# Optimization experiments

Measured on AMD Instinct MI355X. Metric: run time of the kernel, lower is better.

## Reference

```python
import jax, jax.numpy as jnp
import numpy as np
from jax import lax

D = 1024
DI = 2 * D          # mamba inner dim
NS = 16             # ssm state size
DTR = D // 16       # dt rank = 64
KC = 4              # conv kernel
E = 8               # experts
DFF = 2 * D         # expert hidden
TOPK = 2


def _ln(x, g, b):
    mu = x.mean(-1, keepdims=True)
    var = ((x - mu) ** 2).mean(-1, keepdims=True)
    return (x - mu) * lax.rsqrt(var + 1e-5) * g + b


def _silu(x):
    return x * jax.nn.sigmoid(x)


def setup_inputs() -> dict:
    key = jax.random.key(0)
    ks = jax.random.split(key, 20)
    s = 0.02
    inp = {
        "x": jax.random.normal(ks[0], (2, 2048, D), jnp.float32),
        # layernorms
        "ln_mamba_g": jnp.ones((D,), jnp.float32),
        "ln_mamba_b": jnp.zeros((D,), jnp.float32),
        "ln_moe_g": jnp.ones((D,), jnp.float32),
        "ln_moe_b": jnp.zeros((D,), jnp.float32),
        # mamba params
        "in_proj_w": jax.random.normal(ks[1], (2 * DI, D), jnp.float32) * s,
        "in_proj_b": jnp.zeros((2 * DI,), jnp.float32),
        "conv_w": jax.random.normal(ks[2], (DI, KC), jnp.float32) * s,
        "conv_b": jnp.zeros((DI,), jnp.float32),
        "x_proj_w": jax.random.normal(ks[3], (DTR + 2 * NS, DI), jnp.float32) * s,
        "dt_proj_w": jax.random.normal(ks[4], (DI, DTR), jnp.float32) * s,
        "dt_proj_b": jnp.full((DI,), -4.6, jnp.float32),  # softplus -> small dt
        "A_log": jnp.log(jnp.broadcast_to(jnp.arange(1, NS + 1, dtype=jnp.float32), (DI, NS))),
        "D_skip": jnp.ones((DI,), jnp.float32),
        "out_proj_w": jax.random.normal(ks[5], (D, DI), jnp.float32) * s,
        # moe params
        "router_w": jax.random.normal(ks[6], (E, D), jnp.float32) * s,
        "w1": jax.random.normal(ks[7], (E, DFF, D), jnp.float32) * s,
        "b1": jnp.zeros((E, DFF), jnp.float32),
        "w2": jax.random.normal(ks[8], (E, D, DFF), jnp.float32) * s,
        "b2": jnp.zeros((E, D), jnp.float32),
    }
    return inp


def _mamba(x, in_proj_w, in_proj_b, conv_w, conv_b, x_proj_w,
           dt_proj_w, dt_proj_b, A_log, D_skip, out_proj_w):
    Bz, T, _ = x.shape
    xz = x @ in_proj_w.T + in_proj_b            # [B,T,2*DI]
    xi, z = xz[..., :DI], xz[..., DI:]
    # causal depthwise conv, kernel 4
    xp = jnp.pad(xi, ((0, 0), (KC - 1, 0), (0, 0)))
    xc = conv_b + sum(conv_w[:, k] * xp[:, k:k + T, :] for k in range(KC))
    xc = _silu(xc)                              # [B,T,DI]
    proj = xc @ x_proj_w.T                      # [B,T,DTR+2*NS]
    dt_r = proj[..., :DTR]
    Bm = proj[..., DTR:DTR + NS]                # [B,T,NS]
    Cm = proj[..., DTR + NS:]                   # [B,T,NS]
    dt = jax.nn.softplus(dt_r @ dt_proj_w.T + dt_proj_b)  # [B,T,DI]
    A = -jnp.exp(A_log)                         # [DI,NS]

    def step(h, inp):
        xt, dtt, Bt, Ct = inp                   # [B,DI],[B,DI],[B,NS],[B,NS]
        dA = jnp.exp(dtt[:, :, None] * A)       # [B,DI,NS]
        h = dA * h + (dtt * xt)[:, :, None] * Bt[:, None, :]
        y = jnp.einsum('bdn,bn->bd', h, Ct)
        return h, y

    h0 = jnp.zeros((Bz, DI, NS), x.dtype)
    xs = (xc.transpose(1, 0, 2), dt.transpose(1, 0, 2),
          Bm.transpose(1, 0, 2), Cm.transpose(1, 0, 2))
    _, ys = lax.scan(step, h0, xs)              # [T,B,DI]
    y = ys.transpose(1, 0, 2) + xc * D_skip
    y = y * _silu(z)
    return y @ out_proj_w.T                     # [B,T,D]


def _moe(x, router_w, w1, b1, w2, b2):
    logits = x @ router_w.T                     # [B,T,E]
    probs = jax.nn.softmax(logits, axis=-1)
    topv, topi = lax.top_k(probs, TOPK)
    topv = topv / topv.sum(-1, keepdims=True)
    w = (jax.nn.one_hot(topi, E, dtype=x.dtype) * topv[..., None]).sum(-2)  # [B,T,E]
    out = jnp.zeros_like(x)
    for e in range(E):                          # fixed small expert loop
        h1 = _silu(x @ w1[e].T + b1[e])
        ye = h1 @ w2[e].T + b2[e]
        out = out + w[..., e:e + 1] * ye
    return out, {"router_probs": probs}


def reference(x, ln_mamba_g, ln_mamba_b, ln_moe_g, ln_moe_b,
              in_proj_w, in_proj_b, conv_w, conv_b, x_proj_w,
              dt_proj_w, dt_proj_b, A_log, D_skip, out_proj_w,
              router_w, w1, b1, w2, b2):
    h_norm = _ln(x, ln_mamba_g, ln_mamba_b)
    mamba_out = _mamba(h_norm, in_proj_w, in_proj_b, conv_w, conv_b, x_proj_w,
                       dt_proj_w, dt_proj_b, A_log, D_skip, out_proj_w)
    h = x + mamba_out
    h_moe_in = _ln(h, ln_moe_g, ln_moe_b)
    moe_delta, aux = _moe(h_moe_in, router_w, w1, b1, w2, b2)
    h = h + moe_delta
    return (h, aux["router_probs"])
```

## Files before the change

kernel.cpp:

```cpp
#include <hip/hip_runtime.h>
#include <hip/hip_bf16.h>
#include <math.h>

#define NTOK   4096
#define TSEQ   2048
#define DMODEL 1024
#define DINNER 2048
#define NSTATE 16
#define DTRANK 64
#define NEXP   8
#define DFF    2048
#define NCHUNK 32
#define CLEN   64

typedef __attribute__((ext_vector_type(8))) short short8;
typedef __attribute__((ext_vector_type(4))) float f32x4;

__device__ __forceinline__ float fast_rcp(float x){ return __builtin_amdgcn_rcpf(x); }
__device__ __forceinline__ float siluf(float x){ return x * fast_rcp(1.f + __expf(-x)); }

__device__ __forceinline__ unsigned short f2bf(float x){
  unsigned int u = __float_as_uint(x);
  unsigned int r = (u + 0x7FFFu + ((u >> 16) & 1u)) >> 16;
  return (unsigned short)r;
}

__device__ __forceinline__ void split4(float4 a, unsigned short* hi, unsigned short* lo){
  float av[4] = {a.x, a.y, a.z, a.w};
  #pragma unroll
  for (int j=0;j<4;j++){
    unsigned short hu = f2bf(av[j]);
    float hf = __uint_as_float((unsigned int)hu << 16);
    hi[j] = hu;
    lo[j] = f2bf(av[j] - hf);
  }
}

__global__ void zero_kernel(int* __restrict__ p){ p[threadIdx.x] = 0; }

__global__ __launch_bounds__(256) void split_kernel(
    const float* __restrict__ in, unsigned short* __restrict__ hi,
    unsigned short* __restrict__ lo, int n)
{
  int i = (blockIdx.x*256 + threadIdx.x)*4;
  if (i >= n) return;
  float4 v = *(const float4*)(in + i);
  unsigned short ht[4], lt[4];
  split4(v, ht, lt);
  uint2 hw, lw;
  hw.x = (unsigned)ht[0] | ((unsigned)ht[1]<<16);
  hw.y = (unsigned)ht[2] | ((unsigned)ht[3]<<16);
  lw.x = (unsigned)lt[0] | ((unsigned)lt[1]<<16);
  lw.y = (unsigned)lt[2] | ((unsigned)lt[3]<<16);
  *(uint2*)(hi+i) = hw;
  *(uint2*)(lo+i) = lw;
}

__global__ __launch_bounds__(256) void cvt_bf_kernel(
    const float* __restrict__ in, unsigned short* __restrict__ out, int n)
{
  int i = (blockIdx.x*256 + threadIdx.x)*8;
  if (i >= n) return;
  float4 a = *(const float4*)(in+i);
  float4 b = *(const float4*)(in+i+4);
  short8 v;
  v[0]=(short)f2bf(a.x); v[1]=(short)f2bf(a.y); v[2]=(short)f2bf(a.z); v[3]=(short)f2bf(a.w);
  v[4]=(short)f2bf(b.x); v[5]=(short)f2bf(b.y); v[6]=(short)f2bf(b.z); v[7]=(short)f2bf(b.w);
  *(short8*)(out+i) = v;
}

template<int EPI, int BM, bool PS, int CT, bool SK>
__global__ __launch_bounds__(256) void gemm_big(
    const float* __restrict__ A,
    const unsigned short* __restrict__ Ahi, const unsigned short* __restrict__ Alo, int lda,
    const unsigned short* __restrict__ Whi, const unsigned short* __restrict__ Wlo, int ldw,
    int M, int N, int K,
    const float* __restrict__ bias,
    float* __restrict__ out, int ldo)
{
  constexpr int BN  = CT*16;
  constexpr int RG  = BM/64;
  constexpr int TPR = 256/BM;
  constexpr int EA  = 32/TPR;
  constexpr int TPW = 256/BN;
  constexpr int EW  = 32/TPW;
  const int tid = threadIdx.x;
  const int m0 = blockIdx.y * BM;
  const int n0 = blockIdx.x * BN;
  const int koff = SK ? blockIdx.z * K : 0;
  float* outp = out + (SK ? (size_t)blockIdx.z * M * ldo : 0);

  __shared__ __align__(16) unsigned short Ahs[BM*40];
  __shared__ __align__(16) unsigned short Als[BM*40];
  __shared__ __align__(16) unsigned short Whs[BN*40];
  __shared__ __align__(16) unsigned short Wls[BN*40];

  const int arow = tid / TPR;
  const int aseg = (tid % TPR) * EA;
  const int wrow = tid / TPW;
  const int wseg = (tid % TPW) * EW;

  const float* Ap = PS ? nullptr : (A + (size_t)(m0 + arow)*lda + aseg + koff);
  const unsigned short* Aph = PS ? (Ahi + (size_t)(m0 + arow)*lda + aseg + koff) : nullptr;
  const unsigned short* Apl = PS ? (Alo + (size_t)(m0 + arow)*lda + aseg + koff) : nullptr;
  const bool wok = (n0 + wrow) < N;
  const unsigned short* Whp = Whi + (size_t)(n0 + wrow)*ldw + wseg + koff;
  const unsigned short* Wlp = Wlo + (size_t)(n0 + wrow)*ldw + wseg + koff;

  const int lane = tid & 63;
  const int wv   = tid >> 6;
  const int qd   = lane >> 4;
  const int mr   = lane & 15;

  f32x4 acc[RG][CT];
  #pragma unroll
  for (int rg=0; rg<RG; rg++)
    #pragma unroll
    for (int ct=0; ct<CT; ct++) acc[rg][ct] = (f32x4){0.f,0.f,0.f,0.f};

  const unsigned short* ardh = &Ahs[(wv*(16*RG) + mr)*40 + qd*8];
  const unsigned short* ardl = &Als[(wv*(16*RG) + mr)*40 + qd*8];
  const unsigned short* brdh = &Whs[mr*40 + qd*8];
  const unsigned short* brdl = &Wls[mr*40 + qd*8];

  const short8 z8 = {0,0,0,0,0,0,0,0};

  for (int kt = 0; kt < K; kt += 32){
    short8 ah[EA/8], al[EA/8];
    if (PS){
      #pragma unroll
      for (int h=0; h<EA/8; h++){
        ah[h] = *(const short8*)(Aph + kt + h*8);
        al[h] = *(const short8*)(Apl + kt + h*8);
      }
    } else {
      #pragma unroll
      for (int q=0; q<EA/4; q++){
        float4 f = *(const float4*)(Ap + kt + q*4);
        unsigned short ht[4], lt[4];
        split4(f, ht, lt);
        #pragma unroll
        for (int j=0;j<4;j++){
          ah[(q*4+j)/8][(q*4+j)&7] = (short)ht[j];
          al[(q*4+j)/8][(q*4+j)&7] = (short)lt[j];
        }
      }
    }
    short8 wh[EW/8], wl[EW/8];
    #pragma unroll
    for (int h=0; h<EW/8; h++){
      wh[h] = wok ? *(const short8*)(Whp + kt + h*8) : z8;
      wl[h] = wok ? *(const short8*)(Wlp + kt + h*8) : z8;
    }
    __syncthreads();
    #pragma unroll
    for (int h=0; h<EA/8; h++){
      *(short8*)&Ahs[arow*40 + aseg + h*8] = ah[h];
      *(short8*)&Als[arow*40 + aseg + h*8] = al[h];
    }
    #pragma unroll
    for (int h=0; h<EW/8; h++){
      *(short8*)&Whs[wrow*40 + wseg + h*8] = wh[h];
      *(short8*)&Wls[wrow*40 + wseg + h*8] = wl[h];
    }
    __syncthreads();
    #pragma unroll
    for (int rg=0; rg<RG; rg++){
      short8 af = *(const short8*)(ardh + rg*16*40);
      short8 alf= *(const short8*)(ardl + rg*16*40);
      #pragma unroll
      for (int ct=0; ct<CT; ct++){
        short8 bh = *(const short8*)(brdh + ct*16*40);
        short8 bl = *(const short8*)(brdl + ct*16*40);
        f32x4 t = acc[rg][ct];
        t = __builtin_amdgcn_mfma_f32_16x16x32_bf16(af, bh, t, 0,0,0);
        t = __builtin_amdgcn_mfma_f32_16x16x32_bf16(alf, bh, t, 0,0,0);
        t = __builtin_amdgcn_mfma_f32_16x16x32_bf16(af, bl, t, 0,0,0);
        acc[rg][ct] = t;
      }
    }
  }

  #pragma unroll
  for (int rg=0; rg<RG; rg++){
    #pragma unroll
    for (int ct=0; ct<CT; ct++){
      int colg = n0 + ct*16 + mr;
      if (colg >= N) continue;
      float bias_v = (EPI==0 || EPI==2) ? bias[colg] : 0.f;
      #pragma unroll
      for (int r=0;r<4;r++){
        int rowg = m0 + wv*(16*RG) + rg*16 + qd*4 + r;
        float v = acc[rg][ct][r];
        if (EPI == 0){ v += bias_v; }
        else if (EPI == 2){ v += bias_v; v = (v > 20.f) ? v : log1pf(expf(v)); }
        outp[(size_t)rowg*ldo + colg] = v;
      }
    }
  }
}

__global__ __launch_bounds__(256) void reduce4_kernel(
    const float* __restrict__ pp, float* __restrict__ out, int n)
{
  int i = (blockIdx.x*256 + threadIdx.x)*4;
  if (i >= n) return;
  float4 a = *(const float4*)(pp + i);
  float4 b = *(const float4*)(pp + n + i);
  float4 c = *(const float4*)(pp + 2*(size_t)n + i);
  float4 d = *(const float4*)(pp + 3*(size_t)n + i);
  float4 o;
  o.x = (a.x+b.x)+(c.x+d.x);
  o.y = (a.y+b.y)+(c.y+d.y);
  o.z = (a.z+b.z)+(c.z+d.z);
  o.w = (a.w+b.w)+(c.w+d.w);
  *(float4*)(out + i) = o;
}

__global__ __launch_bounds__(256) void reduce2r_kernel(
    const float* __restrict__ p0, const float* __restrict__ p1,
    const float* __restrict__ r, float* __restrict__ out, int n)
{
  int i = (blockIdx.x*256 + threadIdx.x)*4;
  if (i >= n) return;
  float4 a = *(const float4*)(p0 + i);
  float4 b = *(const float4*)(p1 + i);
  float4 c = *(const float4*)(r + i);
  float4 o;
  o.x = a.x+b.x+c.x; o.y = a.y+b.y+c.y; o.z = a.z+b.z+c.z; o.w = a.w+b.w+c.w;
  *(float4*)(out + i) = o;
}

__global__ __launch_bounds__(256) void ln_split_kernel(
    const float* __restrict__ x, const float* __restrict__ g, const float* __restrict__ b,
    unsigned short* __restrict__ hi, unsigned short* __restrict__ lo)
{
  int tok = blockIdx.x;
  int tid = threadIdx.x;
  const float* row = x + (size_t)tok * DMODEL;
  float v[4];
  float s = 0.f, sq = 0.f;
  #pragma unroll
  for (int j=0;j<4;j++){
    v[j] = row[j*256 + tid];
    s += v[j]; sq += v[j]*v[j];
  }
  #pragma unroll
  for (int o=1;o<64;o<<=1){ s += __shfl_xor(s,o,64); sq += __shfl_xor(sq,o,64); }
  __shared__ float ss[4], ssq[4];
  int wid = tid >> 6, lane = tid & 63;
  if (lane == 0){ ss[wid]=s; ssq[wid]=sq; }
  __syncthreads();
  s  = ss[0]+ss[1]+ss[2]+ss[3];
  sq = ssq[0]+ssq[1]+ssq[2]+ssq[3];
  float mu = s * (1.f/DMODEL);
  float var = sq * (1.f/DMODEL) - mu*mu;
  float rs = rsqrtf(var + 1e-5f);
  #pragma unroll
  for (int j=0;j<4;j++){
    int d = j*256 + tid;
    float o = (v[j]-mu)*rs*g[d] + b[d];
    unsigned short hu = f2bf(o);
    float hf = __uint_as_float((unsigned int)hu << 16);
    hi[(size_t)tok*DMODEL + d] = hu;
    lo[(size_t)tok*DMODEL + d] = f2bf(o - hf);
  }
}

__global__ __launch_bounds__(256) void ln2_kernel(
    const float* __restrict__ x, const float* __restrict__ g, const float* __restrict__ b,
    float* __restrict__ out, unsigned short* __restrict__ outb)
{
  int tok = blockIdx.x;
  int tid = threadIdx.x;
  const float* row = x + (size_t)tok * DMODEL;
  float v[4];
  float s = 0.f, sq = 0.f;
  #pragma unroll
  for (int j=0;j<4;j++){
    v[j] = row[j*256 + tid];
    s += v[j]; sq += v[j]*v[j];
  }
  #pragma unroll
  for (int o=1;o<64;o<<=1){ s += __shfl_xor(s,o,64); sq += __shfl_xor(sq,o,64); }
  __shared__ float ss[4], ssq[4];
  int wid = tid >> 6, lane = tid & 63;
  if (lane == 0){ ss[wid]=s; ssq[wid]=sq; }
  __syncthreads();
  s  = ss[0]+ss[1]+ss[2]+ss[3];
  sq = ssq[0]+ssq[1]+ssq[2]+ssq[3];
  float mu = s * (1.f/DMODEL);
  float var = sq * (1.f/DMODEL) - mu*mu;
  float rs = rsqrtf(var + 1e-5f);
  #pragma unroll
  for (int j=0;j<4;j++){
    int d = j*256 + tid;
    float o = (v[j]-mu)*rs*g[d] + b[d];
    out[(size_t)tok*DMODEL + d] = o;
    outb[(size_t)tok*DMODEL + d] = f2bf(o);
  }
}

__global__ __launch_bounds__(256) void conv_kernel(
    const float* __restrict__ xz, const float* __restrict__ cw,
    const float* __restrict__ cb, float* __restrict__ xc)
{
  int i = blockIdx.x*256 + threadIdx.x;
  int tok = i >> 11;
  int ch  = i & 2047;
  int t   = tok & (TSEQ-1);
  int b   = tok >> 11;
  float acc = cb[ch];
  #pragma unroll
  for (int k=0;k<4;k++){
    int tt = t + k - 3;
    if (tt >= 0)
      acc = fmaf(cw[ch*4 + k], xz[(size_t)((b<<11)+tt)*4096 + ch], acc);
  }
  xc[i] = siluf(acc);
}

__global__ __launch_bounds__(256) void scan_partial(
    const float* __restrict__ xz, const float* __restrict__ xc,
    const float* __restrict__ proj, const float* __restrict__ A_log,
    float* __restrict__ P, float* __restrict__ Q)
{
  int tid = threadIdx.x;
  int ch  = blockIdx.x*256 + tid;
  int c   = blockIdx.y;
  int b   = blockIdx.z;
  float A[16];
  #pragma unroll
  for (int n=0;n<16;n++) A[n] = -expf(A_log[ch*NSTATE + n]);
  float h[16];
  #pragma unroll
  for (int n=0;n<16;n++) h[n] = 0.f;
  float sdt = 0.f;
  int tok0 = (b<<11) + c*CLEN;
  float dtv = xz[(size_t)tok0*4096 + ch];
  float xt  = xc[(size_t)tok0*2048 + ch];
  for (int i=0;i<CLEN;i++){
    int tn = tok0 + ((i+1 < CLEN) ? i+1 : i);
    float dtv_n = xz[(size_t)tn*4096 + ch];
    float xt_n  = xc[(size_t)tn*2048 + ch];
    const float4* pB = (const float4*)(proj + (size_t)(tok0+i)*96 + 64);
    float Bv[16];
    *(float4*)&Bv[0]  = pB[0];
    *(float4*)&Bv[4]  = pB[1];
    *(float4*)&Bv[8]  = pB[2];
    *(float4*)&Bv[12] = pB[3];
    float dxt = dtv*xt;
    sdt += dtv;
    #pragma unroll
    for (int n=0;n<16;n++){
      float dA = __expf(dtv*A[n]);
      h[n] = fmaf(dA, h[n], dxt*Bv[n]);
    }
    dtv = dtv_n; xt = xt_n;
  }
  size_t base = ((((size_t)(b*NCHUNK + c))<<11 | ch)<<4);
  #pragma unroll
  for (int n=0;n<16;n++){
    P[base+n] = __expf(A[n]*sdt);
    Q[base+n] = h[n];
  }
}

__global__ __launch_bounds__(256) void scan_combine(
    const float* __restrict__ Q, float* PH)
{
  int g = blockIdx.x*256 + threadIdx.x;
  int n = g & 15, ch = (g>>4) & 2047, b = g>>15;
  float hs = 0.f;
  for (int c=0;c<NCHUNK;c++){
    size_t idx = ((((size_t)(b*NCHUNK + c))<<11 | ch)<<4) | n;
    float pv = PH[idx];
    float qv = Q[idx];
    PH[idx] = hs;
    hs = fmaf(pv, hs, qv);
  }
}

__global__ __launch_bounds__(256) void scan_final(
    const float* __restrict__ xz, float* __restrict__ xc,
    const float* __restrict__ proj, const float* __restrict__ A_log,
    const float* __restrict__ Dskip, const float* __restrict__ Hs)
{
  int tid = threadIdx.x;
  int ch  = blockIdx.x*256 + tid;
  int c   = blockIdx.y;
  int b   = blockIdx.z;
  float A[16];
  #pragma unroll
  for (int n=0;n<16;n++) A[n] = -expf(A_log[ch*NSTATE + n]);
  float Dv = Dskip[ch];
  size_t base = ((((size_t)(b*NCHUNK + c))<<11 | ch)<<4);
  float h[16];
  #pragma unroll
  for (int n=0;n<16;n++) h[n] = Hs[base+n];
  int tok0 = (b<<11) + c*CLEN;
  float dtv = xz[(size_t)tok0*4096 + ch];
  float xt  = xc[(size_t)tok0*2048 + ch];
  float zv  = xz[(size_t)tok0*4096 + 2048 + ch];
  for (int i=0;i<CLEN;i++){
    int tn = tok0 + ((i+1 < CLEN) ? i+1 : i);
    float dtv_n = xz[(size_t)tn*4096 + ch];
    float xt_n  = xc[(size_t)tn*2048 + ch];
    float zv_n  = xz[(size_t)tn*4096 + 2048 + ch];
    const float4* pB = (const float4*)(proj + (size_t)(tok0+i)*96 + 64);
    float Bv[16], Cv[16];
    *(float4*)&Bv[0]  = pB[0];
    *(float4*)&Bv[4]  = pB[1];
    *(float4*)&Bv[8]  = pB[2];
    *(float4*)&Bv[12] = pB[3];
    *(float4*)&Cv[0]  = pB[4];
    *(float4*)&Cv[4]  = pB[5];
    *(float4*)&Cv[8]  = pB[6];
    *(float4*)&Cv[12] = pB[7];
    float dxt = dtv*xt;
    float y = xt*Dv;
    #pragma unroll
    for (int n=0;n<16;n++){
      float dA = __expf(dtv*A[n]);
      h[n] = fmaf(dA, h[n], dxt*Bv[n]);
      y = fmaf(h[n], Cv[n], y);
    }
    xc[(size_t)(tok0+i)*2048 + ch] = y * siluf(zv);
    dtv = dtv_n; xt = xt_n; zv = zv_n;
  }
}

__global__ __launch_bounds__(256) void router_kernel(
    const float* __restrict__ hmoe, const float* __restrict__ rw,
    float* __restrict__ probs_out, int* __restrict__ cnt,
    int* __restrict__ tok_e0, int* __restrict__ tok_e1,
    float* __restrict__ tok_w0, float* __restrict__ tok_w1)
{
  int tok = blockIdx.x;
  int tid = threadIdx.x;
  int e = tid >> 5, l = tid & 31;
  float s = 0.f;
  const float* row = hmoe + (size_t)tok*DMODEL;
  const float* wr  = rw + (size_t)e*DMODEL;
  for (int d=l; d<DMODEL; d+=32) s = fmaf(row[d], wr[d], s);
  #pragma unroll
  for (int o=1;o<32;o<<=1) s += __shfl_xor(s,o,64);
  __shared__ float lg[8];
  if (l==0) lg[e]=s;
  __syncthreads();
  if (tid==0){
    float mx = lg[0];
    for (int k=1;k<8;k++) mx = fmaxf(mx, lg[k]);
    float pe[8]; float den=0.f;
    for (int k=0;k<8;k++){ pe[k]=expf(lg[k]-mx); den+=pe[k]; }
    float inv = 1.f/den;
    for (int k=0;k<8;k++) probs_out[tok*8+k] = pe[k]*inv;
    int i0=0;
    for (int k=1;k<8;k++) if (pe[k] > pe[i0]) i0=k;
    int i1 = (i0==0)?1:0;
    for (int k=0;k<8;k++) if (k!=i0 && pe[k] > pe[i1]) i1=k;
    float v0=pe[i0], v1=pe[i1], sw=v0+v1;
    tok_e0[tok]=i0; tok_e1[tok]=i1;
    tok_w0[tok]=v0/sw; tok_w1[tok]=v1/sw;
    atomicAdd(&cnt[i0],1); atomicAdd(&cnt[i1],1);
  }
}

__global__ void prefix_kernel(const int* cnt, int* off, int* fill){
  if (threadIdx.x==0){
    int s=0;
    for (int e=0;e<NEXP;e++){ off[e]=s; s+=cnt[e]; fill[e]=0; }
  }
}

__global__ __launch_bounds__(256) void fill_kernel(
    const int* tok_e0, const int* tok_e1, const float* tok_w0, const float* tok_w1,
    const int* off, int* fill, int* slot_tok, float* slot_w)
{
  int tok = blockIdx.x*256 + threadIdx.x;
  int e0=tok_e0[tok], e1=tok_e1[tok];
  int p0 = atomicAdd(&fill[e0],1); int s0 = off[e0]+p0;
  slot_tok[s0]=tok; slot_w[s0]=tok_w0[tok];
  int p1 = atomicAdd(&fill[e1],1); int s1 = off[e1]+p1;
  slot_tok[s1]=tok; slot_w[s1]=tok_w1[tok];
}

__global__ __launch_bounds__(256) void moe_gemm1(
    const unsigned short* __restrict__ hnb, const unsigned short* __restrict__ w1b,
    const float* __restrict__ b1,
    const int* __restrict__ cnt, const int* __restrict__ off,
    const int* __restrict__ slot_tok, unsigned short* __restrict__ H1)
{
  int e = blockIdx.z;
  int c = cnt[e];
  int r0 = blockIdx.y*128;
  if (r0 >= c) return;
  int base = off[e];
  int tid = threadIdx.x;
  __shared__ int toks[128];
  if (tid < 128) toks[tid] = (r0 + tid < c) ? slot_tok[base + r0 + tid] : -1;
  __shared__ __align__(16) unsigned short As[128*40];
  __shared__ __align__(16) unsigned short Ws[128*40];
  __syncthreads();

  const int n0   = blockIdx.x*128;
  const int srow = tid >> 1;
  const int sseg = (tid & 1) * 16;
  const int tok  = toks[srow];
  const bool aok = (tok >= 0);
  const unsigned short* Ap = hnb + (size_t)(aok ? tok : 0)*DMODEL + sseg;
  const unsigned short* Wp = w1b + (size_t)e*DFF*DMODEL + (size_t)(n0+srow)*DMODEL + sseg;

  const int lane = tid & 63;
  const int wv   = tid >> 6;
  const int qd   = lane >> 4;
  const int mr   = lane & 15;

  f32x4 acc[2][8];
  #pragma unroll
  for (int rg=0; rg<2; rg++)
    #pragma unroll
    for (int ct=0; ct<8; ct++) acc[rg][ct] = (f32x4){0.f,0.f,0.f,0.f};

  const unsigned short* ard = &As[(wv*32 + mr)*40 + qd*8];
  const unsigned short* brd = &Ws[mr*40 + qd*8];
  const short8 z8 = {0,0,0,0,0,0,0,0};

  for (int kt = 0; kt < DMODEL; kt += 32){
    short8 a0 = aok ? *(const short8*)(Ap + kt)     : z8;
    short8 a1 = aok ? *(const short8*)(Ap + kt + 8) : z8;
    short8 w0 = *(const short8*)(Wp + kt);
    short8 w1v= *(const short8*)(Wp + kt + 8);
    __syncthreads();
    *(short8*)&As[srow*40 + sseg]     = a0;
    *(short8*)&As[srow*40 + sseg + 8] = a1;
    *(short8*)&Ws[srow*40 + sseg]     = w0;
    *(short8*)&Ws[srow*40 + sseg + 8] = w1v;
    __syncthreads();
    #pragma unroll
    for (int rg=0; rg<2; rg++){
      short8 af = *(const short8*)(ard + rg*16*40);
      #pragma unroll
      for (int ct=0; ct<8; ct++){
        short8 bf = *(const short8*)(brd + ct*16*40);
        acc[rg][ct] = __builtin_amdgcn_mfma_f32_16x16x32_bf16(af, bf, acc[rg][ct], 0,0,0);
      }
    }
  }

  #pragma unroll
  for (int rg=0; rg<2; rg++){
    #pragma unroll
    for (int ct=0; ct<8; ct++){
      int colg = n0 + ct*16 + mr;
      float bias = b1[(size_t)e*DFF + colg];
      #pragma unroll
      for (int r=0;r<4;r++){
        int sl = wv*32 + rg*16 + qd*4 + r;
        if (toks[sl] < 0) continue;
        float v = acc[rg][ct][r] + bias;
        H1[(size_t)(base + r0 + sl)*DFF + colg] = f2bf(siluf(v));
      }
    }
  }
}

__global__ __launch_bounds__(256) void moe_gemm2(
    const unsigned short* __restrict__ H1, const unsigned short* __restrict__ w2b,
    const float* __restrict__ b2,
    const int* __restrict__ cnt, const int* __restrict__ off,
    const int* __restrict__ slot_tok, const float* __restrict__ slot_w,
    float* __restrict__ hres)
{
  int e = blockIdx.z;
  int c = cnt[e];
  int r0 = blockIdx.y*128;
  if (r0 >= c) return;
  int base = off[e];
  int tid = threadIdx.x;
  __shared__ int toks[128];
  __shared__ float wts[128];
  if (tid < 128){
    int r = r0 + tid;
    toks[tid] = (r<c) ? slot_tok[base+r] : -1;
    wts[tid]  = (r<c) ? slot_w[base+r] : 0.f;
  }
  __shared__ __align__(16) unsigned short As[128*40];
  __shared__ __align__(16) unsigned short Ws[128*40];
  __syncthreads();

  const int n0   = blockIdx.x*128;
  const int srow = tid >> 1;
  const int sseg = (tid & 1) * 16;
  const bool aok = (toks[srow] >= 0);
  const unsigned short* Ap = H1 + (size_t)(base + r0 + (aok ? srow : 0))*DFF + sseg;
  const unsigned short* Wp = w2b + (size_t)e*DMODEL*DFF + (size_t)(n0+srow)*DFF + sseg;

  const int lane = tid & 63;
  const int wv   = tid >> 6;
  const int qd   = lane >> 4;
  const int mr   = lane & 15;

  f32x4 acc[2][8];
  #pragma unroll
  for (int rg=0; rg<2; rg++)
    #pragma unroll
    for (int ct=0; ct<8; ct++) acc[rg][ct] = (f32x4){0.f,0.f,0.f,0.f};

  const unsigned short* ard = &As[(wv*32 + mr)*40 + qd*8];
  const unsigned short* brd = &Ws[mr*40 + qd*8];
  const short8 z8 = {0,0,0,0,0,0,0,0};

  for (int kt = 0; kt < DFF; kt += 32){
    short8 a0 = aok ? *(const short8*)(Ap + kt)     : z8;
    short8 a1 = aok ? *(const short8*)(Ap + kt + 8) : z8;
    short8 w0 = *(const short8*)(Wp + kt);
    short8 w1v= *(const short8*)(Wp + kt + 8);
    __syncthreads();
    *(short8*)&As[srow*40 + sseg]     = a0;
    *(short8*)&As[srow*40 + sseg + 8] = a1;
    *(short8*)&Ws[srow*40 + sseg]     = w0;
    *(short8*)&Ws[srow*40 + sseg + 8] = w1v;
    __syncthreads();
    #pragma unroll
    for (int rg=0; rg<2; rg++){
      short8 af = *(const short8*)(ard + rg*16*40);
      #pragma unroll
      for (int ct=0; ct<8; ct++){
        short8 bf = *(const short8*)(brd + ct*16*40);
        acc[rg][ct] = __builtin_amdgcn_mfma_f32_16x16x32_bf16(af, bf, acc[rg][ct], 0,0,0);
      }
    }
  }

  #pragma unroll
  for (int rg=0; rg<2; rg++){
    #pragma unroll
    for (int ct=0; ct<8; ct++){
      int colg = n0 + ct*16 + mr;
      float bias = b2[(size_t)e*DMODEL + colg];
      #pragma unroll
      for (int r=0;r<4;r++){
        int sl = wv*32 + rg*16 + qd*4 + r;
        int t = toks[sl];
        if (t < 0) continue;
        float v = acc[rg][ct][r] + bias;
        atomicAdd(&hres[(size_t)t*DMODEL + colg], wts[sl]*v);
      }
    }
  }
}

extern "C" void kernel_launch(void* const* d_in, const int* in_sizes, int n_in,
                              void* d_out, int out_size, void* d_ws, size_t ws_size,
                              hipStream_t stream)
{
  const float* x         = (const float*)d_in[0];
  const float* ln_m_g    = (const float*)d_in[1];
  const float* ln_m_b    = (const float*)d_in[2];
  const float* ln_e_g    = (const float*)d_in[3];
  const float* ln_e_b    = (const float*)d_in[4];
  const float* in_proj_w = (const float*)d_in[5];
  const float* in_proj_b = (const float*)d_in[6];
  const float* conv_w    = (const float*)d_in[7];
  const float* conv_b    = (const float*)d_in[8];
  const float* x_proj_w  = (const float*)d_in[9];
  const float* dt_proj_w = (const float*)d_in[10];
  const float* dt_proj_b = (const float*)d_in[11];
  const float* A_log     = (const float*)d_in[12];
  const float* D_skip    = (const float*)d_in[13];
  const float* out_proj_w= (const float*)d_in[14];
  const float* router_w  = (const float*)d_in[15];
  const float* w1        = (const float*)d_in[16];
  const float* b1        = (const float*)d_in[17];
  const float* w2        = (const float*)d_in[18];
  const float* b2        = (const float*)d_in[19];

  char* ws = (char*)d_ws;
  float* xz   = (float*)(ws + 0);
  float* xc   = (float*)(ws + 67108864ull);
  float* proj = (float*)(ws + 100663296ull);
  char*  misc = ws + 102236160ull;
  float* hn   = (float*)(ws + 0);
  float* pout = (float*)(ws + 16777216ull);
  unsigned short* H1    = (unsigned short*)(ws + 16777216ull);
  unsigned short* hn_bf = (unsigned short*)(ws + 50331648ull);
  unsigned short* wmoe  = (unsigned short*)(ws + 67108864ull);

  unsigned short* hn_hi = (unsigned short*)d_out;
  unsigned short* hn_lo = hn_hi + 4194304;
  float* Pbuf = (float*)d_out;
  float* Qbuf = (float*)d_out + (2u<<20);
  float* ppx  = (float*)((char*)d_out + 2097152ull);

  unsigned short* Wi_hi = (unsigned short*)(ws + 67108864ull);
  unsigned short* Wi_lo = Wi_hi + 4194304;
  unsigned short* Wo_hi = (unsigned short*)Qbuf;
  unsigned short* Wo_lo = Wo_hi + 2097152;
  unsigned short* Wx_hi = (unsigned short*)d_out;
  unsigned short* Wx_lo = Wx_hi + 196608;
  unsigned short* Wd_hi = Wx_lo + 196608;
  unsigned short* Wd_lo = Wd_hi + 131072;

  int*   cnt      = (int*)(misc);
  int*   fill     = (int*)(misc + 64);
  int*   offp     = (int*)(misc + 128);
  int*   tok_e0   = (int*)(misc + 1024);
  int*   tok_e1   = (int*)(misc + 1024 + 16384);
  float* tok_w0   = (float*)(misc + 1024 + 32768);
  float* tok_w1   = (float*)(misc + 1024 + 49152);
  int*   slot_tok = (int*)(misc + 1024 + 65536);
  float* slot_w   = (float*)(misc + 1024 + 98304);
  float* out_h    = (float*)d_out;
  float* probs_out= (float*)d_out + 4194304;

  zero_kernel<<<1, 64, 0, stream>>>(cnt);

  split_kernel<<<4096, 256, 0, stream>>>(in_proj_w, Wi_hi, Wi_lo, 4194304);
  ln_split_kernel<<<NTOK, 256, 0, stream>>>(x, ln_m_g, ln_m_b, hn_hi, hn_lo);
  gemm_big<0,128,true,8,false><<<dim3(32, 32), 256, 0, stream>>>(
      nullptr, hn_hi, hn_lo, DMODEL, Wi_hi, Wi_lo, DMODEL, NTOK, 4096, DMODEL,
      in_proj_b, xz, 4096);
  split_kernel<<<192, 256, 0, stream>>>(x_proj_w, Wx_hi, Wx_lo, 196608);
  split_kernel<<<128, 256, 0, stream>>>(dt_proj_w, Wd_hi, Wd_lo, 131072);
  conv_kernel<<<NTOK*DINNER/256, 256, 0, stream>>>(xz, conv_w, conv_b, xc);
  gemm_big<1,64,false,8,true><<<dim3(1, 64, 4), 256, 0, stream>>>(
      xc, nullptr, nullptr, DINNER, Wx_hi, Wx_lo, DINNER, NTOK, 96, 512,
      nullptr, ppx, 96);
  reduce4_kernel<<<384, 256, 0, stream>>>(ppx, proj, NTOK*96);
  gemm_big<2,128,false,8,false><<<dim3(16, 32), 256, 0, stream>>>(
      proj, nullptr, nullptr, 96, Wd_hi, Wd_lo, DTRANK, NTOK, DINNER, DTRANK,
      dt_proj_b, xz, 4096);
  scan_partial<<<dim3(DINNER/256, NCHUNK, 2), 256, 0, stream>>>(
      xz, xc, proj, A_log, Pbuf, Qbuf);
  scan_combine<<<256, 256, 0, stream>>>(Qbuf, Pbuf);
  scan_final<<<dim3(DINNER/256, NCHUNK, 2), 256, 0, stream>>>(
      xz, xc, proj, A_log, D_skip, Pbuf);
  split_kernel<<<2048, 256, 0, stream>>>(out_proj_w, Wo_hi, Wo_lo, 2097152);
  gemm_big<1,128,false,8,true><<<dim3(8, 32, 2), 256, 0, stream>>>(
      xc, nullptr, nullptr, DINNER, Wo_hi, Wo_lo, DINNER, NTOK, DMODEL, 1024,
      nullptr, pout, DMODEL);
  reduce2r_kernel<<<4096, 256, 0, stream>>>(pout, pout + 4194304, x, out_h,
                                            NTOK*DMODEL);

  ln2_kernel<<<NTOK, 256, 0, stream>>>(out_h, ln_e_g, ln_e_b, hn, hn_bf);
  router_kernel<<<NTOK, 256, 0, stream>>>(hn, router_w, probs_out, cnt,
                                          tok_e0, tok_e1, tok_w0, tok_w1);
  prefix_kernel<<<1, 64, 0, stream>>>(cnt, offp, fill);
  fill_kernel<<<NTOK/256, 256, 0, stream>>>(tok_e0, tok_e1, tok_w0, tok_w1,
                                            offp, fill, slot_tok, slot_w);
  cvt_bf_kernel<<<8192, 256, 0, stream>>>(w1, wmoe, NEXP*DFF*DMODEL);
  moe_gemm1<<<dim3(DFF/128, 32, NEXP), 256, 0, stream>>>(
      hn_bf, wmoe, b1, cnt, offp, slot_tok, H1);
  cvt_bf_kernel<<<8192, 256, 0, stream>>>(w2, wmoe, NEXP*DMODEL*DFF);
  moe_gemm2<<<dim3(DMODEL/128, 32, NEXP), 256, 0, stream>>>(
      H1, wmoe, b2, cnt, offp, slot_tok, slot_w, out_h);
}
```

Baseline: 968.0 us.

## Double-buffer shared-memory tiles in dense and MoE GEMM kernels

Converts the main GEMM and both MoE expert GEMM kernels from single-buffered LDS tiles to double buffering. The next K-tile's global loads are issued before the MFMA loop on the current tile and stored into the alternate buffer afterwards, which cuts one barrier per iteration. This is meant to hide global-load latency behind matrix math. In exchange it doubles LDS per block and keeps the prefetched registers live across the MFMA loop, which can lower occupancy.

```diff
diff --git a/kernel.cpp b/kernel.cpp
--- a/kernel.cpp
+++ b/kernel.cpp
@@ -84,16 +84,18 @@
   constexpr int EA  = 32/TPR;
   constexpr int TPW = 256/BN;
   constexpr int EW  = 32/TPW;
+  constexpr int AH  = BM*40;
+  constexpr int WH  = BN*40;
   const int tid = threadIdx.x;
   const int m0 = blockIdx.y * BM;
   const int n0 = blockIdx.x * BN;
   const int koff = SK ? blockIdx.z * K : 0;
   float* outp = out + (SK ? (size_t)blockIdx.z * M * ldo : 0);
 
-  __shared__ __align__(16) unsigned short Ahs[BM*40];
-  __shared__ __align__(16) unsigned short Als[BM*40];
-  __shared__ __align__(16) unsigned short Whs[BN*40];
-  __shared__ __align__(16) unsigned short Wls[BN*40];
+  __shared__ __align__(16) unsigned short Ahs[2*AH];
+  __shared__ __align__(16) unsigned short Als[2*AH];
+  __shared__ __align__(16) unsigned short Whs[2*WH];
+  __shared__ __align__(16) unsigned short Wls[2*WH];
 
   const int arow = tid / TPR;
   const int aseg = (tid % TPR) * EA;
@@ -118,15 +120,13 @@
     #pragma unroll
     for (int ct=0; ct<CT; ct++) acc[rg][ct] = (f32x4){0.f,0.f,0.f,0.f};
 
-  const unsigned short* ardh = &Ahs[(wv*(16*RG) + mr)*40 + qd*8];
-  const unsigned short* ardl = &Als[(wv*(16*RG) + mr)*40 + qd*8];
-  const unsigned short* brdh = &Whs[mr*40 + qd*8];
-  const unsigned short* brdl = &Wls[mr*40 + qd*8];
-
+  const int ard_o = (wv*(16*RG) + mr)*40 + qd*8;
+  const int brd_o = mr*40 + qd*8;
   const short8 z8 = {0,0,0,0,0,0,0,0};
 
-  for (int kt = 0; kt < K; kt += 32){
-    short8 ah[EA/8], al[EA/8];
+  short8 ah[EA/8], al[EA/8], wh[EW/8], wl[EW/8];
+
+  auto load_tile = [&](int kt){
     if (PS){
       #pragma unroll
       for (int h=0; h<EA/8; h++){
@@ -146,32 +146,41 @@
         }
       }
     }
-    short8 wh[EW/8], wl[EW/8];
     #pragma unroll
     for (int h=0; h<EW/8; h++){
       wh[h] = wok ? *(const short8*)(Whp + kt + h*8) : z8;
       wl[h] = wok ? *(const short8*)(Wlp + kt + h*8) : z8;
     }
-    __syncthreads();
+  };
+  auto store_tile = [&](int b){
     #pragma unroll
     for (int h=0; h<EA/8; h++){
-      *(short8*)&Ahs[arow*40 + aseg + h*8] = ah[h];
-      *(short8*)&Als[arow*40 + aseg + h*8] = al[h];
+      *(short8*)&Ahs[b*AH + arow*40 + aseg + h*8] = ah[h];
+      *(short8*)&Als[b*AH + arow*40 + aseg + h*8] = al[h];
     }
     #pragma unroll
     for (int h=0; h<EW/8; h++){
-      *(short8*)&Whs[wrow*40 + wseg + h*8] = wh[h];
-      *(short8*)&Wls[wrow*40 + wseg + h*8] = wl[h];
-    }
-    __syncthreads();
+      *(short8*)&Whs[b*WH + wrow*40 + wseg + h*8] = wh[h];
+      *(short8*)&Wls[b*WH + wrow*40 + wseg + h*8] = wl[h];
+    }
+  };
+
+  load_tile(0);
+  store_tile(0);
+  __syncthreads();
+
+  int cur = 0;
+  for (int kt = 0; kt < K; kt += 32){
+    const bool hn = (kt + 32 < K);
+    if (hn) load_tile(kt + 32);
     #pragma unroll
     for (int rg=0; rg<RG; rg++){
-      short8 af = *(const short8*)(ardh + rg*16*40);
-      short8 alf= *(const short8*)(ardl + rg*16*40);
+      short8 af = *(const short8*)&Ahs[cur*AH + ard_o + rg*16*40];
+      short8 alf= *(const short8*)&Als[cur*AH + ard_o + rg*16*40];
       #pragma unroll
       for (int ct=0; ct<CT; ct++){
-        short8 bh = *(const short8*)(brdh + ct*16*40);
-        short8 bl = *(const short8*)(brdl + ct*16*40);
+        short8 bh = *(const short8*)&Whs[cur*WH + brd_o + ct*16*40];
+        short8 bl = *(const short8*)&Wls[cur*WH + brd_o + ct*16*40];
         f32x4 t = acc[rg][ct];
         t = __builtin_amdgcn_mfma_f32_16x16x32_bf16(af, bh, t, 0,0,0);
         t = __builtin_amdgcn_mfma_f32_16x16x32_bf16(alf, bh, t, 0,0,0);
@@ -179,6 +188,9 @@
         acc[rg][ct] = t;
       }
     }
+    if (hn) store_tile(cur ^ 1);
+    __syncthreads();
+    cur ^= 1;
   }
 
   #pragma unroll
@@ -499,8 +511,8 @@
   int tid = threadIdx.x;
   __shared__ int toks[128];
   if (tid < 128) toks[tid] = (r0 + tid < c) ? slot_tok[base + r0 + tid] : -1;
-  __shared__ __align__(16) unsigned short As[128*40];
-  __shared__ __align__(16) unsigned short Ws[128*40];
+  __shared__ __align__(16) unsigned short As[2*128*40];
+  __shared__ __align__(16) unsigned short Ws[2*128*40];
   __syncthreads();
 
   const int n0   = blockIdx.x*128;
@@ -522,30 +534,44 @@
     #pragma unroll
     for (int ct=0; ct<8; ct++) acc[rg][ct] = (f32x4){0.f,0.f,0.f,0.f};
 
-  const unsigned short* ard = &As[(wv*32 + mr)*40 + qd*8];
-  const unsigned short* brd = &Ws[mr*40 + qd*8];
+  const int ard_o = (wv*32 + mr)*40 + qd*8;
+  const int brd_o = mr*40 + qd*8;
   const short8 z8 = {0,0,0,0,0,0,0,0};
-
+  constexpr int HB = 128*40;
+
+  short8 a0, a1, w0, w1v;
+  auto load_tile = [&](int kt){
+    a0 = aok ? *(const short8*)(Ap + kt)     : z8;
+    a1 = aok ? *(const short8*)(Ap + kt + 8) : z8;
+    w0 = *(const short8*)(Wp + kt);
+    w1v= *(const short8*)(Wp + kt + 8);
+  };
+  auto store_tile = [&](int b){
+    *(short8*)&As[b*HB + srow*40 + sseg]     = a0;
+    *(short8*)&As[b*HB + srow*40 + sseg + 8] = a1;
+    *(short8*)&Ws[b*HB + srow*40 + sseg]     = w0;
+    *(short8*)&Ws[b*HB + srow*40 + sseg + 8] = w1v;
+  };
+
+  load_tile(0);
+  store_tile(0);
+  __syncthreads();
+  int cur = 0;
   for (int kt = 0; kt < DMODEL; kt += 32){
-    short8 a0 = aok ? *(const short8*)(Ap + kt)     : z8;
-    short8 a1 = aok ? *(const short8*)(Ap + kt + 8) : z8;
-    short8 w0 = *(const short8*)(Wp + kt);
-    short8 w1v= *(const short8*)(Wp + kt + 8);
-    __syncthreads();
-    *(short8*)&As[srow*40 + sseg]     = a0;
-    *(short8*)&As[srow*40 + sseg + 8] = a1;
-    *(short8*)&Ws[srow*40 + sseg]     = w0;
-    *(short8*)&Ws[srow*40 + sseg + 8] = w1v;
-    __syncthreads();
+    const bool hn = (kt + 32 < DMODEL);
+    if (hn) load_tile(kt + 32);
     #pragma unroll
     for (int rg=0; rg<2; rg++){
-      short8 af = *(const short8*)(ard + rg*16*40);
+      short8 af = *(const short8*)&As[cur*HB + ard_o + rg*16*40];
       #pragma unroll
       for (int ct=0; ct<8; ct++){
-        short8 bf = *(const short8*)(brd + ct*16*40);
+        short8 bf = *(const short8*)&Ws[cur*HB + brd_o + ct*16*40];
         acc[rg][ct] = __builtin_amdgcn_mfma_f32_16x16x32_bf16(af, bf, acc[rg][ct], 0,0,0);
       }
     }
+    if (hn) store_tile(cur ^ 1);
+    __syncthreads();
+    cur ^= 1;
   }
 
   #pragma unroll
@@ -585,8 +611,8 @@
     toks[tid] = (r<c) ? slot_tok[base+r] : -1;
     wts[tid]  = (r<c) ? slot_w[base+r] : 0.f;
   }
-  __shared__ __align__(16) unsigned short As[128*40];
-  __shared__ __align__(16) unsigned short Ws[128*40];
+  __shared__ __align__(16) unsigned short As[2*128*40];
+  __shared__ __align__(16) unsigned short Ws[2*128*40];
   __syncthreads();
 
   const int n0   = blockIdx.x*128;
@@ -607,30 +633,44 @@
     #pragma unroll
     for (int ct=0; ct<8; ct++) acc[rg][ct] = (f32x4){0.f,0.f,0.f,0.f};
 
-  const unsigned short* ard = &As[(wv*32 + mr)*40 + qd*8];
-  const unsigned short* brd = &Ws[mr*40 + qd*8];
+  const int ard_o = (wv*32 + mr)*40 + qd*8;
+  const int brd_o = mr*40 + qd*8;
   const short8 z8 = {0,0,0,0,0,0,0,0};
-
+  constexpr int HB = 128*40;
+
+  short8 a0, a1, w0, w1v;
+  auto load_tile = [&](int kt){
+    a0 = aok ? *(const short8*)(Ap + kt)     : z8;
+    a1 = aok ? *(const short8*)(Ap + kt + 8) : z8;
+    w0 = *(const short8*)(Wp + kt);
+    w1v= *(const short8*)(Wp + kt + 8);
+  };
+  auto store_tile = [&](int b){
+    *(short8*)&As[b*HB + srow*40 + sseg]     = a0;
+    *(short8*)&As[b*HB + srow*40 + sseg + 8] = a1;
+    *(short8*)&Ws[b*HB + srow*40 + sseg]     = w0;
+    *(short8*)&Ws[b*HB + srow*40 + sseg + 8] = w1v;
+  };
+
+  load_tile(0);
+  store_tile(0);
+  __syncthreads();
+  int cur = 0;
   for (int kt = 0; kt < DFF; kt += 32){
-    short8 a0 = aok ? *(const short8*)(Ap + kt)     : z8;
-    short8 a1 = aok ? *(const short8*)(Ap + kt + 8) : z8;
-    short8 w0 = *(const short8*)(Wp + kt);
-    short8 w1v= *(const short8*)(Wp + kt + 8);
-    __syncthreads();
-    *(short8*)&As[srow*40 + sseg]     = a0;
-    *(short8*)&As[srow*40 + sseg + 8] = a1;
-    *(short8*)&Ws[srow*40 + sseg]     = w0;
-    *(short8*)&Ws[srow*40 + sseg + 8] = w1v;
-    __syncthreads();
+    const bool hn = (kt + 32 < DFF);
+    if (hn) load_tile(kt + 32);
     #pragma unroll
     for (int rg=0; rg<2; rg++){
-      short8 af = *(const short8*)(ard + rg*16*40);
+      short8 af = *(const short8*)&As[cur*HB + ard_o + rg*16*40];
       #pragma unroll
       for (int ct=0; ct<8; ct++){
-        short8 bf = *(const short8*)(brd + ct*16*40);
+        short8 bf = *(const short8*)&Ws[cur*HB + brd_o + ct*16*40];
         acc[rg][ct] = __builtin_amdgcn_mfma_f32_16x16x32_bf16(af, bf, acc[rg][ct], 0,0,0);
       }
     }
+    if (hn) store_tile(cur ^ 1);
+    __syncthreads();
+    cur ^= 1;
   }
 
   #pragma unroll
```

After: 936.2 us. -3.3%, faster.
